# Kernel optimization log

Hardware: AMD Instinct MI355X
Metric: run time of the kernel (lower is better)

## Reference

```python
import jax, jax.numpy as jnp
import numpy as np

NUM_HEADS = 4
HEAD_DIM = 64
BN_EPS = 1e-5

def _leaky_relu(x, slope=0.2):
    return jnp.where(x >= 0, x, slope * x)

def _gat_conv(x, W, a_src, a_dst, src, dst):
    # x: [N, F_in], W: [F_out, F_in], a_*: [H, D]; edges src/dst: [E]
    N = x.shape[0]
    h = (x @ W.T).reshape(N, NUM_HEADS, HEAD_DIM)          # [N, H, D]
    s_src = jnp.einsum('nhd,hd->nh', h, a_src)              # [N, H]
    s_dst = jnp.einsum('nhd,hd->nh', h, a_dst)              # [N, H]
    e = _leaky_relu(s_src[src] + s_dst[dst])                # [E, H]
    # segment softmax over edges grouped by dst; torch index_reduce_ starts
    # from zeros (include_self=True) -> max with 0
    e_max = jnp.maximum(jax.ops.segment_max(e, dst, num_segments=N), 0.0)
    e_exp = jnp.exp(e - e_max[dst])                         # [E, H]
    e_sum = jax.ops.segment_sum(e_exp, dst, num_segments=N) # [N, H]
    alpha = e_exp / jnp.maximum(e_sum[dst], 1e-9)           # [E, H]
    msg = h[src] * alpha[..., None]                         # [E, H, D]
    out = jax.ops.segment_sum(msg, dst, num_segments=N)     # [N, H, D]
    return out.reshape(N, NUM_HEADS * HEAD_DIM)

def _bn_eval(x, gamma, beta, mean, var):
    return (x - mean) * jax.lax.rsqrt(var + BN_EPS) * gamma + beta

def _elu(x):
    return jnp.where(x > 0, x, jnp.expm1(x))

def setup_inputs() -> dict:
    key = jax.random.key(0)
    ks = jax.random.split(key, 12)
    N, E, IN, HID, OUT = 50000, 500000, 256, 256, 64
    s = 0.05
    return {
        'x': jax.random.normal(ks[0], (N, IN), jnp.float32),
        'edge_index': jax.random.randint(ks[1], (2, E), 0, N, jnp.int64),
        'W1': jax.random.normal(ks[2], (HID, IN), jnp.float32) * s,
        'a_src1': jax.random.normal(ks[3], (NUM_HEADS, HEAD_DIM), jnp.float32) * s,
        'a_dst1': jax.random.normal(ks[4], (NUM_HEADS, HEAD_DIM), jnp.float32) * s,
        'bn1_gamma': jnp.ones((HID,), jnp.float32),
        'bn1_beta': jnp.zeros((HID,), jnp.float32),
        'bn1_mean': jnp.zeros((HID,), jnp.float32),
        'bn1_var': jnp.ones((HID,), jnp.float32),
        'W2': jax.random.normal(ks[5], (HID, HID), jnp.float32) * s,
        'a_src2': jax.random.normal(ks[6], (NUM_HEADS, HEAD_DIM), jnp.float32) * s,
        'a_dst2': jax.random.normal(ks[7], (NUM_HEADS, HEAD_DIM), jnp.float32) * s,
        'bn2_gamma': jnp.ones((HID,), jnp.float32),
        'bn2_beta': jnp.zeros((HID,), jnp.float32),
        'bn2_mean': jnp.zeros((HID,), jnp.float32),
        'bn2_var': jnp.ones((HID,), jnp.float32),
        'Wc': jax.random.normal(ks[8], (OUT, HID), jnp.float32) * s,
        'bc': jnp.zeros((OUT,), jnp.float32),
    }

def reference(x, edge_index, W1, a_src1, a_dst1, bn1_gamma, bn1_beta, bn1_mean, bn1_var,
              W2, a_src2, a_dst2, bn2_gamma, bn2_beta, bn2_mean, bn2_var, Wc, bc):
    src, dst = edge_index[0], edge_index[1]
    h = _gat_conv(x, W1, a_src1, a_dst1, src, dst)
    h = _elu(_bn_eval(h, bn1_gamma, bn1_beta, bn1_mean, bn1_var))
    h = _gat_conv(h, W2, a_src2, a_dst2, src, dst)
    h = _elu(_bn_eval(h, bn2_gamma, bn2_beta, bn2_mean, bn2_var))
    return h @ Wc.T + bc
```

## Files before the change

kernel.cpp:

```cpp
#include <hip/hip_runtime.h>

typedef __attribute__((ext_vector_type(8))) short short8;
typedef __attribute__((ext_vector_type(4))) float f32x4;

#define FF 256
#define NHEAD 4
#define HDIM 64
#define LDS_PITCH 264

__device__ __forceinline__ float bf2f(unsigned short u) {
  union { unsigned u; float f; } v; v.u = ((unsigned)u) << 16; return v.f;
}
__device__ __forceinline__ unsigned short f2bf(float f) {
  union { unsigned u; float f; } v; v.f = f;
  unsigned r = v.u + 0x7FFFu + ((v.u >> 16) & 1u);
  return (unsigned short)(r >> 16);
}

__global__ __launch_bounds__(256) void cvt4z_kernel(
    const float* __restrict__ p0, int n0, const float* __restrict__ p1, int n1,
    const float* __restrict__ p2, int n2, const float* __restrict__ p3, int n3,
    unsigned short* __restrict__ o0, unsigned short* __restrict__ o1,
    unsigned short* __restrict__ o2, unsigned short* __restrict__ o3,
    int* __restrict__ deg, int nz4) {
  int i = blockIdx.x * 256 + threadIdx.x;
  const float* in;
  unsigned short* out;
  int idx;
  if (i < n0) { in = p0; out = o0; idx = i; }
  else if (i < n0 + n1) { in = p1; out = o1; idx = i - n0; }
  else if (i < n0 + n1 + n2) { in = p2; out = o2; idx = i - n0 - n1; }
  else if (i < n0 + n1 + n2 + n3) { in = p3; out = o3; idx = i - n0 - n1 - n2; }
  else {
    int z = i - n0 - n1 - n2 - n3;
    if (z < nz4) ((int4*)deg)[z] = int4{0, 0, 0, 0};
    return;
  }
  f32x4 v = ((const f32x4*)in)[idx];
  ushort4 o;
  o.x = f2bf(v.x); o.y = f2bf(v.y); o.z = f2bf(v.z); o.w = f2bf(v.w);
  ((ushort4*)out)[idx] = o;
}

__global__ void hist_kernel(const int* __restrict__ dst, int* __restrict__ deg,
                            int E, int N) {
  int i = blockIdx.x * blockDim.x + threadIdx.x;
  if (i < E) {
    int d = dst[i];
    if ((unsigned)d < (unsigned)N) atomicAdd(&deg[d], 1);
  }
}

__global__ __launch_bounds__(256) void scan_chunks(const int* __restrict__ deg,
                                                   int* __restrict__ excl,
                                                   int* __restrict__ csum, int N) {
  __shared__ int s[256];
  int t = threadIdx.x;
  int base = blockIdx.x * 1024 + t * 4;
  int v[4];
  int sum = 0;
#pragma unroll
  for (int i = 0; i < 4; ++i) {
    v[i] = (base + i < N) ? deg[base + i] : 0;
    sum += v[i];
  }
  s[t] = sum;
  __syncthreads();
  for (int off = 1; off < 256; off <<= 1) {
    int x = (t >= off) ? s[t - off] : 0;
    __syncthreads();
    s[t] += x;
    __syncthreads();
  }
  int run = s[t] - sum;
#pragma unroll
  for (int i = 0; i < 4; ++i) {
    if (base + i < N) excl[base + i] = run;
    run += v[i];
  }
  if (t == 255) csum[blockIdx.x] = s[255];
}

__global__ void finalize_rows(const int* __restrict__ excl, const int* __restrict__ csum,
                              int* __restrict__ row_start, int* __restrict__ cursor,
                              int N, int E) {
  int i = blockIdx.x * blockDim.x + threadIdx.x;
  if (i < N) {
    int chunk = i >> 10;
    int pre = 0;
    for (int k = 0; k < chunk; ++k) pre += csum[k];
    int v = excl[i] + pre;
    row_start[i] = v;
    cursor[i] = v;
  }
  if (i == 0) row_start[N] = E;
}

__global__ void scatter_kernel(const int* __restrict__ src, const int* __restrict__ dst,
                               int* __restrict__ cursor, int* __restrict__ sorted_src,
                               int E, int N) {
  int i = blockIdx.x * blockDim.x + threadIdx.x;
  if (i < E) {
    int d = dst[i];
    int s = src[i];
    if ((unsigned)d < (unsigned)N) {
      int p = atomicAdd(&cursor[d], 1);
      if ((unsigned)p < (unsigned)E)
        sorted_src[p] = ((unsigned)s < (unsigned)N) ? s : 0;
    }
  }
}

__global__ __launch_bounds__(256) void gemm_main(const unsigned short* __restrict__ A,
                                                 const unsigned short* __restrict__ B,
                                                 unsigned short* __restrict__ Cb,
                                                 const float* __restrict__ a_src,
                                                 const float* __restrict__ a_dst,
                                                 float* __restrict__ sS,
                                                 float* __restrict__ sD,
                                                 int M) {
  __shared__ unsigned short Atile[64 * LDS_PITCH];
  const int K = 256;
  int tid = threadIdx.x;
  int wave = tid >> 6;
  int lane = tid & 63;
  int row0w = blockIdx.x * 64;
  int col0 = wave * 64;
  int lr = lane & 15;
  int quad = lane >> 4;

  short8 breg[4][8];
  {
    const unsigned short* Bp0 = B + (size_t)(col0 + lr) * K + quad * 8;
#pragma unroll
    for (int t = 0; t < 4; ++t)
#pragma unroll
      for (int kk = 0; kk < 8; ++kk)
        breg[t][kk] = *(const short8*)(Bp0 + (size_t)(16 * t) * K + kk * 32);
  }

  {
    short8 stg[8];
#pragma unroll
    for (int pass = 0; pass < 8; ++pass) {
      int c = tid + pass * 256;
      int row = c >> 5;
      int col8 = (c & 31) * 8;
      int grow = row0w + row;
      if (grow >= M) grow = M - 1;
      stg[pass] = *(const short8*)(A + (size_t)grow * K + col8);
    }
#pragma unroll
    for (int pass = 0; pass < 8; ++pass) {
      int c = tid + pass * 256;
      int row = c >> 5;
      int col8 = (c & 31) * 8;
      *(short8*)(&Atile[row * LDS_PITCH + col8]) = stg[pass];
    }
  }
  __syncthreads();

  f32x4 acc[4][4];
#pragma unroll
  for (int rt = 0; rt < 4; ++rt)
#pragma unroll
    for (int t = 0; t < 4; ++t) acc[rt][t] = f32x4{0, 0, 0, 0};

#pragma unroll
  for (int kk = 0; kk < 8; ++kk) {
    short8 a[4];
#pragma unroll
    for (int rt = 0; rt < 4; ++rt)
      a[rt] = *(const short8*)(&Atile[(rt * 16 + lr) * LDS_PITCH + quad * 8 + kk * 32]);
#pragma unroll
    for (int rt = 0; rt < 4; ++rt)
#pragma unroll
      for (int t = 0; t < 4; ++t)
        acc[rt][t] = __builtin_amdgcn_mfma_f32_16x16x32_bf16(a[rt], breg[t][kk], acc[rt][t], 0, 0, 0);
  }

#pragma unroll
  for (int rt = 0; rt < 4; ++rt) {
#pragma unroll
    for (int t = 0; t < 4; ++t) {
#pragma unroll
      for (int r = 0; r < 4; ++r) {
        int row = row0w + rt * 16 + quad * 4 + r;
        if (row < M) {
          int col = col0 + 16 * t + lr;
          Cb[(size_t)row * FF + col] = f2bf(acc[rt][t][r]);
        }
      }
    }
  }

  {
    float asv[4], adv[4];
#pragma unroll
    for (int t = 0; t < 4; ++t) {
      asv[t] = a_src[col0 + 16 * t + lr];
      adv[t] = a_dst[col0 + 16 * t + lr];
    }
#pragma unroll
    for (int rt = 0; rt < 4; ++rt) {
#pragma unroll
      for (int r = 0; r < 4; ++r) {
        float ps = acc[rt][0][r] * asv[0] + acc[rt][1][r] * asv[1] +
                   acc[rt][2][r] * asv[2] + acc[rt][3][r] * asv[3];
        float pd = acc[rt][0][r] * adv[0] + acc[rt][1][r] * adv[1] +
                   acc[rt][2][r] * adv[2] + acc[rt][3][r] * adv[3];
#pragma unroll
        for (int sft = 1; sft < 16; sft <<= 1) {
          ps += __shfl_xor(ps, sft);
          pd += __shfl_xor(pd, sft);
        }
        if (lr == 0) {
          int row = row0w + rt * 16 + quad * 4 + r;
          if (row < M) {
            sS[row * NHEAD + wave] = ps;
            sD[row * NHEAD + wave] = pd;
          }
        }
      }
    }
  }
}

__global__ __launch_bounds__(256) void gemm_head(const unsigned short* __restrict__ A,
                                                 const unsigned short* __restrict__ B,
                                                 float* __restrict__ Cf,
                                                 const float* __restrict__ bias,
                                                 int M) {
  const int K = 256;
  int wave = threadIdx.x >> 6;
  int lane = threadIdx.x & 63;
  int row0w = blockIdx.x * 256 + wave * 64;
  if (row0w >= M) return;
  int lr = lane & 15;
  int quad = lane >> 4;

  short8 breg[4][8];
  {
    const unsigned short* Bp0 = B + (size_t)lr * K + quad * 8;
#pragma unroll
    for (int t = 0; t < 4; ++t)
#pragma unroll
      for (int kk = 0; kk < 8; ++kk)
        breg[t][kk] = *(const short8*)(Bp0 + (size_t)(16 * t) * K + kk * 32);
  }

  const unsigned short* Aps[4];
#pragma unroll
  for (int rt = 0; rt < 4; ++rt) {
    int arow = row0w + rt * 16 + lr;
    if (arow >= M) arow = M - 1;
    Aps[rt] = A + (size_t)arow * K + quad * 8;
  }

  f32x4 acc[4][4];
#pragma unroll
  for (int rt = 0; rt < 4; ++rt)
#pragma unroll
    for (int t = 0; t < 4; ++t) acc[rt][t] = f32x4{0, 0, 0, 0};

#pragma unroll
  for (int kk = 0; kk < 8; ++kk) {
    short8 a[4];
#pragma unroll
    for (int rt = 0; rt < 4; ++rt) a[rt] = *(const short8*)(Aps[rt] + kk * 32);
#pragma unroll
    for (int rt = 0; rt < 4; ++rt)
#pragma unroll
      for (int t = 0; t < 4; ++t)
        acc[rt][t] = __builtin_amdgcn_mfma_f32_16x16x32_bf16(a[rt], breg[t][kk], acc[rt][t], 0, 0, 0);
  }

#pragma unroll
  for (int rt = 0; rt < 4; ++rt) {
#pragma unroll
    for (int t = 0; t < 4; ++t) {
#pragma unroll
      for (int r = 0; r < 4; ++r) {
        int row = row0w + rt * 16 + quad * 4 + r;
        if (row < M) {
          int col = 16 * t + lr;
          Cf[(size_t)row * 64 + col] = acc[rt][t][r] + bias[col];
        }
      }
    }
  }
}

__global__ __launch_bounds__(256) void aggregate_kernel(
    const unsigned short* __restrict__ hprev, const float* __restrict__ sS,
    const float* __restrict__ sD, const int* __restrict__ row_start,
    const int* __restrict__ sorted_src, const float* __restrict__ gamma,
    const float* __restrict__ beta, const float* __restrict__ mean,
    const float* __restrict__ var, unsigned short* __restrict__ hout, int N) {
  int wave = threadIdx.x >> 6;
  int lane = threadIdx.x & 63;
  int n = blockIdx.x * 4 + wave;
  if (n >= N) return;
  int hh = lane >> 4;
  int slot = lane & 15;
  int f0 = lane * 4;
  int srcBase = lane & 48;
  int jb = row_start[n];
  int je = row_start[n + 1];
  int jlast = je - 1;
  float sdv = sD[n * NHEAD + hh];
  float l = 0.f;
  float o0 = 0.f, o1 = 0.f, o2 = 0.f, o3 = 0.f;

  for (int c = jb; c < je; c += 16) {
    int j = c + slot;
    int jc = (j < jlast) ? j : jlast;
    int s = sorted_src[jc];
    float e = sS[s * NHEAD + hh] + sdv;
    e = (e >= 0.f) ? e : 0.2f * e;
    float w = (j < je) ? __expf(e) : 0.f;
    l += w;

    {
      uint2 u[8];
#pragma unroll
      for (int k = 0; k < 8; ++k) {
        int sk = __shfl(s, srcBase + k, 64);
        u[k] = *(const uint2*)(hprev + (size_t)sk * FF + f0);
      }
#pragma unroll
      for (int k = 0; k < 8; ++k) {
        float a = __shfl(w, srcBase + k, 64);
        o0 += a * __uint_as_float(u[k].x << 16);
        o1 += a * __uint_as_float(u[k].x & 0xffff0000u);
        o2 += a * __uint_as_float(u[k].y << 16);
        o3 += a * __uint_as_float(u[k].y & 0xffff0000u);
      }
    }
    if (c + 8 < je) {
      uint2 u[8];
#pragma unroll
      for (int k = 8; k < 16; ++k) {
        int sk = __shfl(s, srcBase + k, 64);
        u[k - 8] = *(const uint2*)(hprev + (size_t)sk * FF + f0);
      }
#pragma unroll
      for (int k = 8; k < 16; ++k) {
        float a = __shfl(w, srcBase + k, 64);
        o0 += a * __uint_as_float(u[k - 8].x << 16);
        o1 += a * __uint_as_float(u[k - 8].x & 0xffff0000u);
        o2 += a * __uint_as_float(u[k - 8].y << 16);
        o3 += a * __uint_as_float(u[k - 8].y & 0xffff0000u);
      }
    }
  }

  l += __shfl_xor(l, 1);
  l += __shfl_xor(l, 2);
  l += __shfl_xor(l, 4);
  l += __shfl_xor(l, 8);
  float li = 1.f / fmaxf(l, 1e-9f);

  f32x4 g = *(const f32x4*)(gamma + f0);
  f32x4 b = *(const f32x4*)(beta + f0);
  f32x4 mu = *(const f32x4*)(mean + f0);
  f32x4 vr = *(const f32x4*)(var + f0);
  float v0 = (o0 * li - mu.x) * rsqrtf(vr.x + 1e-5f) * g.x + b.x;
  float v1 = (o1 * li - mu.y) * rsqrtf(vr.y + 1e-5f) * g.y + b.y;
  float v2 = (o2 * li - mu.z) * rsqrtf(vr.z + 1e-5f) * g.z + b.z;
  float v3 = (o3 * li - mu.w) * rsqrtf(vr.w + 1e-5f) * g.w + b.w;
  v0 = (v0 > 0.f) ? v0 : expm1f(v0);
  v1 = (v1 > 0.f) ? v1 : expm1f(v1);
  v2 = (v2 > 0.f) ? v2 : expm1f(v2);
  v3 = (v3 > 0.f) ? v3 : expm1f(v3);
  ushort4 ov;
  ov.x = f2bf(v0); ov.y = f2bf(v1); ov.z = f2bf(v2); ov.w = f2bf(v3);
  *(ushort4*)(hout + (size_t)n * FF + f0) = ov;
}

extern "C" void kernel_launch(void* const* d_in, const int* in_sizes, int n_in,
                              void* d_out, int out_size, void* d_ws, size_t ws_size,
                              hipStream_t stream) {
  const float* x   = (const float*)d_in[0];
  const int* ei    = (const int*)d_in[1];
  const float* W1  = (const float*)d_in[2];
  const float* as1 = (const float*)d_in[3];
  const float* ad1 = (const float*)d_in[4];
  const float* g1  = (const float*)d_in[5];
  const float* b1  = (const float*)d_in[6];
  const float* m1  = (const float*)d_in[7];
  const float* v1  = (const float*)d_in[8];
  const float* W2  = (const float*)d_in[9];
  const float* as2 = (const float*)d_in[10];
  const float* ad2 = (const float*)d_in[11];
  const float* g2  = (const float*)d_in[12];
  const float* b2  = (const float*)d_in[13];
  const float* m2  = (const float*)d_in[14];
  const float* v2  = (const float*)d_in[15];
  const float* Wc  = (const float*)d_in[16];
  const float* bc  = (const float*)d_in[17];

  const int N = in_sizes[0] / FF;
  const int E = in_sizes[1] / 2;
  const int* srcIdx = ei;
  const int* dstIdx = ei + E;

  char* ws = (char*)d_ws;
  size_t off = 0;
  auto take = [&](size_t bytes) -> void* {
    void* p = ws + off;
    off += (bytes + 255) & ~(size_t)255;
    return p;
  };
  int* deg        = (int*)take((size_t)N * 4);
  int* excl       = (int*)take((size_t)N * 4);
  int* csum       = (int*)take(256 * 4);
  int* row_start  = (int*)take(((size_t)N + 1) * 4);
  int* cursor     = (int*)take((size_t)N * 4);
  int* sorted_src = (int*)take((size_t)E * 4);
  float* sS       = (float*)take((size_t)N * NHEAD * 4);
  float* sD       = (float*)take((size_t)N * NHEAD * 4);
  unsigned short* hpre = (unsigned short*)take((size_t)N * FF * 2);
  unsigned short* hact = (unsigned short*)take((size_t)N * FF * 2);
  unsigned short* xb   = (unsigned short*)take((size_t)N * FF * 2);
  unsigned short* w1b  = (unsigned short*)take((size_t)FF * FF * 2);
  unsigned short* w2b  = (unsigned short*)take((size_t)FF * FF * 2);
  unsigned short* wcb  = (unsigned short*)take((size_t)64 * FF * 2);

  const int tpb = 256;

  {
    int n0 = (N * FF) / 4, n1 = (FF * FF) / 4, n2 = (FF * FF) / 4, n3 = (64 * FF) / 4;
    int nz4 = (N + 3) / 4;
    int tot = n0 + n1 + n2 + n3 + nz4;
    cvt4z_kernel<<<(tot + tpb - 1) / tpb, tpb, 0, stream>>>(x, n0, W1, n1, W2, n2, Wc, n3,
                                                            xb, w1b, w2b, wcb, deg, nz4);
  }

  hist_kernel<<<(E + tpb - 1) / tpb, tpb, 0, stream>>>(dstIdx, deg, E, N);
  int nchunks = (N + 1023) / 1024;
  scan_chunks<<<nchunks, 256, 0, stream>>>(deg, excl, csum, N);
  finalize_rows<<<(N + tpb - 1) / tpb, tpb, 0, stream>>>(excl, csum, row_start, cursor, N, E);
  scatter_kernel<<<(E + tpb - 1) / tpb, tpb, 0, stream>>>(srcIdx, dstIdx, cursor, sorted_src, E, N);

  int aggBlocks = (N + 3) / 4;
  int gemmBlocks = (N + 63) / 64;
  int headBlocks = (N + 255) / 256;

  gemm_main<<<gemmBlocks, 256, 0, stream>>>(xb, w1b, hpre, as1, ad1, sS, sD, N);
  aggregate_kernel<<<aggBlocks, 256, 0, stream>>>(hpre, sS, sD, row_start, sorted_src,
                                                  g1, b1, m1, v1, hact, N);
  gemm_main<<<gemmBlocks, 256, 0, stream>>>(hact, w2b, hpre, as2, ad2, sS, sD, N);
  aggregate_kernel<<<aggBlocks, 256, 0, stream>>>(hpre, sS, sD, row_start, sorted_src,
                                                  g2, b2, m2, v2, hact, N);
  gemm_head<<<headBlocks, 256, 0, stream>>>(hact, wcb, (float*)d_out, bc, N);
}
```

Measured before the change: 346.2 us.

## Fuse fp32-to-bf16 conversion of x into first GEMM and batch aggregate gathers

The separate conversion pass that wrote a bf16 copy of x is removed. The first GEMM is now templated to read fp32 rows and convert them while staging into LDS, which saves one full write and reread of the N×256 input. The aggregate kernel now issues all 16 neighbor gathers before doing the FMAs, so more loads are in flight at once, at the cost of more registers. The GEMM staging loop also stores each load to LDS straight away instead of buffering all eight loads first, which may expose more load latency.

```diff
diff --git a/kernel.cpp b/kernel.cpp
--- a/kernel.cpp
+++ b/kernel.cpp
@@ -17,12 +17,25 @@
   return (unsigned short)(r >> 16);
 }
 
-__global__ __launch_bounds__(256) void cvt4z_kernel(
+__device__ __forceinline__ short8 loadA8(const unsigned short* p) {
+  return *(const short8*)p;
+}
+__device__ __forceinline__ short8 loadA8(const float* p) {
+  f32x4 a = *(const f32x4*)p;
+  f32x4 b = *(const f32x4*)(p + 4);
+  short8 r;
+  r[0] = (short)f2bf(a.x); r[1] = (short)f2bf(a.y);
+  r[2] = (short)f2bf(a.z); r[3] = (short)f2bf(a.w);
+  r[4] = (short)f2bf(b.x); r[5] = (short)f2bf(b.y);
+  r[6] = (short)f2bf(b.z); r[7] = (short)f2bf(b.w);
+  return r;
+}
+
+__global__ __launch_bounds__(256) void cvtw_kernel(
     const float* __restrict__ p0, int n0, const float* __restrict__ p1, int n1,
-    const float* __restrict__ p2, int n2, const float* __restrict__ p3, int n3,
+    const float* __restrict__ p2, int n2,
     unsigned short* __restrict__ o0, unsigned short* __restrict__ o1,
-    unsigned short* __restrict__ o2, unsigned short* __restrict__ o3,
-    int* __restrict__ deg, int nz4) {
+    unsigned short* __restrict__ o2, int* __restrict__ deg, int nz4) {
   int i = blockIdx.x * 256 + threadIdx.x;
   const float* in;
   unsigned short* out;
@@ -30,9 +43,8 @@
   if (i < n0) { in = p0; out = o0; idx = i; }
   else if (i < n0 + n1) { in = p1; out = o1; idx = i - n0; }
   else if (i < n0 + n1 + n2) { in = p2; out = o2; idx = i - n0 - n1; }
-  else if (i < n0 + n1 + n2 + n3) { in = p3; out = o3; idx = i - n0 - n1 - n2; }
   else {
-    int z = i - n0 - n1 - n2 - n3;
+    int z = i - n0 - n1 - n2;
     if (z < nz4) ((int4*)deg)[z] = int4{0, 0, 0, 0};
     return;
   }
@@ -111,7 +123,8 @@
   }
 }
 
-__global__ __launch_bounds__(256) void gemm_main(const unsigned short* __restrict__ A,
+template <typename AT>
+__global__ __launch_bounds__(256) void gemm_main(const AT* __restrict__ A,
                                                  const unsigned short* __restrict__ B,
                                                  unsigned short* __restrict__ Cb,
                                                  const float* __restrict__ a_src,
@@ -140,7 +153,6 @@
   }
 
   {
-    short8 stg[8];
 #pragma unroll
     for (int pass = 0; pass < 8; ++pass) {
       int c = tid + pass * 256;
@@ -148,14 +160,8 @@
       int col8 = (c & 31) * 8;
       int grow = row0w + row;
       if (grow >= M) grow = M - 1;
-      stg[pass] = *(const short8*)(A + (size_t)grow * K + col8);
-    }
-#pragma unroll
-    for (int pass = 0; pass < 8; ++pass) {
-      int c = tid + pass * 256;
-      int row = c >> 5;
-      int col8 = (c & 31) * 8;
-      *(short8*)(&Atile[row * LDS_PITCH + col8]) = stg[pass];
+      short8 v = loadA8(A + (size_t)grow * K + col8);
+      *(short8*)(&Atile[row * LDS_PITCH + col8]) = v;
     }
   }
   __syncthreads();
@@ -321,36 +327,36 @@
     float w = (j < je) ? __expf(e) : 0.f;
     l += w;
 
-    {
-      uint2 u[8];
-#pragma unroll
-      for (int k = 0; k < 8; ++k) {
+    bool b2 = (c + 8 < je);
+    uint2 u[16];
+#pragma unroll
+    for (int k = 0; k < 8; ++k) {
+      int sk = __shfl(s, srcBase + k, 64);
+      u[k] = *(const uint2*)(hprev + (size_t)sk * FF + f0);
+    }
+    if (b2) {
+#pragma unroll
+      for (int k = 8; k < 16; ++k) {
         int sk = __shfl(s, srcBase + k, 64);
         u[k] = *(const uint2*)(hprev + (size_t)sk * FF + f0);
       }
-#pragma unroll
-      for (int k = 0; k < 8; ++k) {
+    }
+#pragma unroll
+    for (int k = 0; k < 8; ++k) {
+      float a = __shfl(w, srcBase + k, 64);
+      o0 += a * __uint_as_float(u[k].x << 16);
+      o1 += a * __uint_as_float(u[k].x & 0xffff0000u);
+      o2 += a * __uint_as_float(u[k].y << 16);
+      o3 += a * __uint_as_float(u[k].y & 0xffff0000u);
+    }
+    if (b2) {
+#pragma unroll
+      for (int k = 8; k < 16; ++k) {
         float a = __shfl(w, srcBase + k, 64);
         o0 += a * __uint_as_float(u[k].x << 16);
         o1 += a * __uint_as_float(u[k].x & 0xffff0000u);
         o2 += a * __uint_as_float(u[k].y << 16);
         o3 += a * __uint_as_float(u[k].y & 0xffff0000u);
-      }
-    }
-    if (c + 8 < je) {
-      uint2 u[8];
-#pragma unroll
-      for (int k = 8; k < 16; ++k) {
-        int sk = __shfl(s, srcBase + k, 64);
-        u[k - 8] = *(const uint2*)(hprev + (size_t)sk * FF + f0);
-      }
-#pragma unroll
-      for (int k = 8; k < 16; ++k) {
-        float a = __shfl(w, srcBase + k, 64);
-        o0 += a * __uint_as_float(u[k - 8].x << 16);
-        o1 += a * __uint_as_float(u[k - 8].x & 0xffff0000u);
-        o2 += a * __uint_as_float(u[k - 8].y << 16);
-        o3 += a * __uint_as_float(u[k - 8].y & 0xffff0000u);
       }
     }
   }
@@ -412,7 +418,7 @@
     off += (bytes + 255) & ~(size_t)255;
     return p;
   };
-  int* deg        = (int*)take((size_t)N * 4);
+  int* deg        = (int*)take((size_t)((N + 3) & ~3) * 4);
   int* excl       = (int*)take((size_t)N * 4);
   int* csum       = (int*)take(256 * 4);
   int* row_start  = (int*)take(((size_t)N + 1) * 4);
@@ -422,7 +428,6 @@
   float* sD       = (float*)take((size_t)N * NHEAD * 4);
   unsigned short* hpre = (unsigned short*)take((size_t)N * FF * 2);
   unsigned short* hact = (unsigned short*)take((size_t)N * FF * 2);
-  unsigned short* xb   = (unsigned short*)take((size_t)N * FF * 2);
   unsigned short* w1b  = (unsigned short*)take((size_t)FF * FF * 2);
   unsigned short* w2b  = (unsigned short*)take((size_t)FF * FF * 2);
   unsigned short* wcb  = (unsigned short*)take((size_t)64 * FF * 2);
@@ -430,11 +435,11 @@
   const int tpb = 256;
 
   {
-    int n0 = (N * FF) / 4, n1 = (FF * FF) / 4, n2 = (FF * FF) / 4, n3 = (64 * FF) / 4;
+    int n0 = (FF * FF) / 4, n1 = (FF * FF) / 4, n2 = (64 * FF) / 4;
     int nz4 = (N + 3) / 4;
-    int tot = n0 + n1 + n2 + n3 + nz4;
-    cvt4z_kernel<<<(tot + tpb - 1) / tpb, tpb, 0, stream>>>(x, n0, W1, n1, W2, n2, Wc, n3,
-                                                            xb, w1b, w2b, wcb, deg, nz4);
+    int tot = n0 + n1 + n2 + nz4;
+    cvtw_kernel<<<(tot + tpb - 1) / tpb, tpb, 0, stream>>>(W1, n0, W2, n1, Wc, n2,
+                                                           w1b, w2b, wcb, deg, nz4);
   }
 
   hist_kernel<<<(E + tpb - 1) / tpb, tpb, 0, stream>>>(dstIdx, deg, E, N);
@@ -447,10 +452,11 @@
   int gemmBlocks = (N + 63) / 64;
   int headBlocks = (N + 255) / 256;
 
-  gemm_main<<<gemmBlocks, 256, 0, stream>>>(xb, w1b, hpre, as1, ad1, sS, sD, N);
+  gemm_main<float><<<gemmBlocks, 256, 0, stream>>>(x, w1b, hpre, as1, ad1, sS, sD, N);
   aggregate_kernel<<<aggBlocks, 256, 0, stream>>>(hpre, sS, sD, row_start, sorted_src,
                                                   g1, b1, m1, v1, hact, N);
-  gemm_main<<<gemmBlocks, 256, 0, stream>>>(hact, w2b, hpre, as2, ad2, sS, sD, N);
+  gemm_main<unsigned short><<<gemmBlocks, 256, 0, stream>>>(hact, w2b, hpre, as2, ad2,
+                                                            sS, sD, N);
   aggregate_kernel<<<aggBlocks, 256, 0, stream>>>(hpre, sS, sD, row_start, sorted_src,
                                                   g2, b2, m2, v2, hact, N);
   gemm_head<<<headBlocks, 256, 0, stream>>>(hact, wcb, (float*)d_out, bc, N);
```

Result: slower. 359.6 us (+3.9%).
